# Kernel tuning notes

Measured on AMD Instinct MI355X. Metric: run time of the kernel, lower is better.

The kernel has to match this reference:

```python
import jax, jax.numpy as jnp
import numpy as np
from jax import lax

KERNELS = (3, 5, 7, 9, 11, 13, 15)
H = W = 4096


def _box_mean(x, k):
    """2D box-mean filter with replicate (edge) padding, computed separably.

    Edge padding is separable, so (pad2d -> kxk box) == (padH -> kx1 box -> padW -> 1xk box).
    x: [N, 1, H, W]
    """
    p = k // 2
    kh = jnp.full((1, 1, k, 1), 1.0 / k, dtype=x.dtype)
    kw = jnp.full((1, 1, 1, k), 1.0 / k, dtype=x.dtype)
    dn = ('NCHW', 'OIHW', 'NCHW')
    y = jnp.pad(x, ((0, 0), (0, 0), (p, p), (0, 0)), mode='edge')
    y = lax.conv_general_dilated(y, kh, (1, 1), 'VALID', dimension_numbers=dn)
    y = jnp.pad(y, ((0, 0), (0, 0), (0, 0), (p, p)), mode='edge')
    y = lax.conv_general_dilated(y, kw, (1, 1), 'VALID', dimension_numbers=dn)
    return y


def setup_inputs() -> dict:
    key = jax.random.key(0)
    k1, k2 = jax.random.split(key)
    x = jax.random.uniform(k1, (1, 1, H, W), dtype=jnp.float32)
    # binary occupancy-style map, as float (torch uses mapU8 -> fp16 multiply)
    map_mask = (jax.random.uniform(k2, (H, W)) > 0.5).astype(jnp.float32)
    return {"x": x, "map_mask": map_mask}


def reference(x, map_mask):
    # sum of 7 multi-scale box means, averaged, then masked by the map
    acc = _box_mean(x, KERNELS[0])
    for k in KERNELS[1:]:
        acc = acc + _box_mean(x, k)
    out = acc / len(KERNELS)
    return out * map_mask[None, None, :, :]
```

## Files before the change

kernel.cpp:

```cpp
#include <hip/hip_runtime.h>


#define TILE   64
#define HALO   7
#define LHX    8
#define NCOL   80
#define NROW   78
#define PSTR   83
#define PROWSA 81
#define HH     4096
#define WW     4096

__global__ __launch_bounds__(256, 8) void meanconv_kernel(
    const float* __restrict__ x, const float* __restrict__ mask,
    float* __restrict__ out)
{
    __shared__ float P[PROWSA * PSTR];
    const int tid = threadIdx.x;

    const int lid  = blockIdx.x;
    const int tile = ((lid & 7) << 9) | (lid >> 3);
    const int c0   = (tile & 63) * TILE;
    const int r0   = (tile >> 6) * TILE;

    const int g  = tid & 7;
    const int ty = tid >> 3;
    const int B0 = 8 * g;
    const size_t mrow0 = (size_t)(r0 + ty) * WW + c0 + B0;
    const size_t mrow1 = (size_t)(r0 + ty + 32) * WW + c0 + B0;
    float4 mk[4];
    mk[0] = *(const float4*)&mask[mrow0];
    mk[1] = *(const float4*)&mask[mrow0 + 4];
    mk[2] = *(const float4*)&mask[mrow1];
    mk[3] = *(const float4*)&mask[mrow1 + 4];

    if (tid < 81) P[tid] = 0.0f;

    const bool xint = (c0 >= LHX) && (c0 - LHX + NCOL <= WW);

    for (int idx = tid; idx < NROW * 4; idx += 256) {
        const int lr  = idx >> 2;
        const int s   = idx & 3;
        const int gr  = min(max(r0 + lr - HALO, 0), HH - 1);
        const int gc0 = c0 - LHX + 20 * s;
        float v[20];
        if (xint) {
            const float* src = &x[(size_t)gr * WW + gc0];
            #pragma unroll
            for (int q = 0; q < 5; ++q) {
                const float4 t = *(const float4*)(src + 4 * q);
                v[4*q+0] = t.x; v[4*q+1] = t.y; v[4*q+2] = t.z; v[4*q+3] = t.w;
            }
        } else {
            #pragma unroll
            for (int i = 0; i < 20; ++i) {
                const int gc = min(max(gc0 + i, 0), WW - 1);
                v[i] = x[(size_t)gr * WW + gc];
            }
        }
        #pragma unroll
        for (int i = 1; i < 20; ++i) v[i] += v[i - 1];
        const float tot = v[19];
        float sum = tot;
        float u = __shfl_up(sum, 1, 4); if (s >= 1) sum += u;
        u       = __shfl_up(sum, 2, 4); if (s >= 2) sum += u;
        const float off = sum - tot;
        float* dst = &P[(lr + 1) * PSTR + 1 + 20 * s];
        #pragma unroll
        for (int i = 0; i < 20; ++i) dst[i] = v[i] + off;
    }
    __syncthreads();

    for (int idx = tid; idx < 80 * 4; idx += 256) {
        const int c  = (idx >> 2) + 1;
        const int s  = idx & 3;
        const int rs = 1 + 20 * s;
        float v[20];
        float run = 0.0f;
        #pragma unroll
        for (int i = 0; i < 20; ++i) {
            const int r = rs + i;
            float t = P[r * PSTR + c];
            t = (r < 79) ? t : 0.0f;
            run += t; v[i] = run;
        }
        const float tot = run;
        float sum = tot;
        float u = __shfl_up(sum, 1, 4); if (s >= 1) sum += u;
        u       = __shfl_up(sum, 2, 4); if (s >= 2) sum += u;
        const float off = sum - tot;
        #pragma unroll
        for (int i = 0; i < 20; ++i) {
            const int r = rs + i;
            if (r < 79) P[r * PSTR + c] = v[i] + off;
        }
    }
    __syncthreads();

    #pragma unroll
    for (int j = 0; j < 2; ++j) {
        const int rr = ty + 32 * j;
        const int A  = rr + HALO;
        float a[8] = {0.f,0.f,0.f,0.f,0.f,0.f,0.f,0.f};
        #pragma unroll
        for (int p = 1; p <= 7; ++p) {
            const int   k = 2 * p + 1;
            const float w = 1.0f / (7.0f * (float)(k * k));
            const float* rT = &P[(A - p) * PSTR];
            const float* rB = &P[(A + p + 1) * PSTR];
            const int cl = B0 + LHX - p;
            const int cr = cl + 2 * p + 1;
            #pragma unroll
            for (int i = 0; i < 8; ++i) {
                a[i] += w * (rB[cr + i] - rT[cr + i] - rB[cl + i] + rT[cl + i]);
            }
        }
        const int gr = r0 + rr, gc = c0 + B0;
        const float4 m0 = mk[2 * j];
        const float4 m1 = mk[2 * j + 1];
        float4 o0, o1;
        o0.x = a[0] * m0.x; o0.y = a[1] * m0.y; o0.z = a[2] * m0.z; o0.w = a[3] * m0.w;
        o1.x = a[4] * m1.x; o1.y = a[5] * m1.y; o1.z = a[6] * m1.z; o1.w = a[7] * m1.w;
        *(float4*)&out[(size_t)gr * WW + gc]     = o0;
        *(float4*)&out[(size_t)gr * WW + gc + 4] = o1;
    }
}

extern "C" void kernel_launch(void* const* d_in, const int* in_sizes, int n_in,
                              void* d_out, int out_size, void* d_ws, size_t ws_size,
                              hipStream_t stream) {
    const float* x    = (const float*)d_in[0];
    const float* mask = (const float*)d_in[1];
    float*       out  = (float*)d_out;
    meanconv_kernel<<<dim3(64 * 64), 256, 0, stream>>>(x, mask, out);
}
```

Measured before the change: 207.1 us.

## Split integral-image scans into two segments per row/column and defer mask loads

The row and column prefix-sum passes switch from four 20-element segments per line to two 40/39-element segments. This drops one shuffle level and the loop striding, and shrinks the shared buffer by removing the leading zero column. The column pass recomputes from shared memory instead of holding a 20-element register array. Mask loads move from the kernel start to the epilogue, which lowers register pressure but exposes their latency and leaves fewer threads active during the scan phases.

```diff
diff --git a/kernel.cpp b/kernel.cpp
--- a/kernel.cpp
+++ b/kernel.cpp
@@ -7,7 +7,7 @@
 #define NCOL   80
 #define NROW   78
 #define PSTR   83
-#define PROWSA 81
+#define PROWS  79
 #define HH     4096
 #define WW     4096
 
@@ -15,7 +15,7 @@
     const float* __restrict__ x, const float* __restrict__ mask,
     float* __restrict__ out)
 {
-    __shared__ float P[PROWSA * PSTR];
+    __shared__ float P[PROWS * PSTR];
     const int tid = threadIdx.x;
 
     const int lid  = blockIdx.x;
@@ -23,80 +23,62 @@
     const int c0   = (tile & 63) * TILE;
     const int r0   = (tile >> 6) * TILE;
 
-    const int g  = tid & 7;
-    const int ty = tid >> 3;
-    const int B0 = 8 * g;
-    const size_t mrow0 = (size_t)(r0 + ty) * WW + c0 + B0;
-    const size_t mrow1 = (size_t)(r0 + ty + 32) * WW + c0 + B0;
-    float4 mk[4];
-    mk[0] = *(const float4*)&mask[mrow0];
-    mk[1] = *(const float4*)&mask[mrow0 + 4];
-    mk[2] = *(const float4*)&mask[mrow1];
-    mk[3] = *(const float4*)&mask[mrow1 + 4];
-
-    if (tid < 81) P[tid] = 0.0f;
+    if (tid < PSTR) P[tid] = 0.0f;
 
     const bool xint = (c0 >= LHX) && (c0 - LHX + NCOL <= WW);
 
-    for (int idx = tid; idx < NROW * 4; idx += 256) {
-        const int lr  = idx >> 2;
-        const int s   = idx & 3;
+    if (tid < NROW * 2) {
+        const int lr  = tid >> 1;
+        const int s   = tid & 1;
         const int gr  = min(max(r0 + lr - HALO, 0), HH - 1);
-        const int gc0 = c0 - LHX + 20 * s;
-        float v[20];
+        const int gc0 = c0 - LHX + 40 * s;
+        float v[40];
         if (xint) {
             const float* src = &x[(size_t)gr * WW + gc0];
             #pragma unroll
-            for (int q = 0; q < 5; ++q) {
+            for (int q = 0; q < 10; ++q) {
                 const float4 t = *(const float4*)(src + 4 * q);
                 v[4*q+0] = t.x; v[4*q+1] = t.y; v[4*q+2] = t.z; v[4*q+3] = t.w;
             }
         } else {
             #pragma unroll
-            for (int i = 0; i < 20; ++i) {
+            for (int i = 0; i < 40; ++i) {
                 const int gc = min(max(gc0 + i, 0), WW - 1);
                 v[i] = x[(size_t)gr * WW + gc];
             }
         }
         #pragma unroll
-        for (int i = 1; i < 20; ++i) v[i] += v[i - 1];
-        const float tot = v[19];
-        float sum = tot;
-        float u = __shfl_up(sum, 1, 4); if (s >= 1) sum += u;
-        u       = __shfl_up(sum, 2, 4); if (s >= 2) sum += u;
-        const float off = sum - tot;
-        float* dst = &P[(lr + 1) * PSTR + 1 + 20 * s];
+        for (int i = 1; i < 40; ++i) v[i] += v[i - 1];
+        const float tot = v[39];
+        const float u   = __shfl_up(tot, 1, 2);
+        const float off = (s == 1) ? u : 0.0f;
+        float* dst = &P[(lr + 1) * PSTR + 40 * s];
         #pragma unroll
-        for (int i = 0; i < 20; ++i) dst[i] = v[i] + off;
+        for (int i = 0; i < 40; ++i) dst[i] = v[i] + off;
     }
     __syncthreads();
 
-    for (int idx = tid; idx < 80 * 4; idx += 256) {
-        const int c  = (idx >> 2) + 1;
-        const int s  = idx & 3;
-        const int rs = 1 + 20 * s;
-        float v[20];
+    if (tid < NCOL * 2) {
+        const int c  = tid >> 1;
+        const int s  = tid & 1;
+        const int rs = 1 + 39 * s;
         float run = 0.0f;
         #pragma unroll
-        for (int i = 0; i < 20; ++i) {
-            const int r = rs + i;
-            float t = P[r * PSTR + c];
-            t = (r < 79) ? t : 0.0f;
-            run += t; v[i] = run;
-        }
-        const float tot = run;
-        float sum = tot;
-        float u = __shfl_up(sum, 1, 4); if (s >= 1) sum += u;
-        u       = __shfl_up(sum, 2, 4); if (s >= 2) sum += u;
-        const float off = sum - tot;
+        for (int i = 0; i < 39; ++i) run += P[(rs + i) * PSTR + c];
+        const float u   = __shfl_up(run, 1, 2);
+        const float off = (s == 1) ? u : 0.0f;
+        float acc = off;
         #pragma unroll
-        for (int i = 0; i < 20; ++i) {
-            const int r = rs + i;
-            if (r < 79) P[r * PSTR + c] = v[i] + off;
+        for (int i = 0; i < 39; ++i) {
+            acc += P[(rs + i) * PSTR + c];
+            P[(rs + i) * PSTR + c] = acc;
         }
     }
     __syncthreads();
 
+    const int g  = tid & 7;
+    const int ty = tid >> 3;
+    const int B0 = 8 * g;
     #pragma unroll
     for (int j = 0; j < 2; ++j) {
         const int rr = ty + 32 * j;
@@ -108,16 +90,16 @@
             const float w = 1.0f / (7.0f * (float)(k * k));
             const float* rT = &P[(A - p) * PSTR];
             const float* rB = &P[(A + p + 1) * PSTR];
-            const int cl = B0 + LHX - p;
-            const int cr = cl + 2 * p + 1;
+            const int cl = B0 + 7 - p;
+            const int cr = B0 + 8 + p;
             #pragma unroll
             for (int i = 0; i < 8; ++i) {
-                a[i] += w * (rB[cr + i] - rT[cr + i] - rB[cl + i] + rT[cl + i]);
+                a[i] += w * ((rB[cr + i] - rT[cr + i]) - (rB[cl + i] - rT[cl + i]));
             }
         }
         const int gr = r0 + rr, gc = c0 + B0;
-        const float4 m0 = mk[2 * j];
-        const float4 m1 = mk[2 * j + 1];
+        const float4 m0 = *(const float4*)&mask[(size_t)gr * WW + gc];
+        const float4 m1 = *(const float4*)&mask[(size_t)gr * WW + gc + 4];
         float4 o0, o1;
         o0.x = a[0] * m0.x; o0.y = a[1] * m0.y; o0.z = a[2] * m0.z; o0.w = a[3] * m0.w;
         o1.x = a[4] * m1.x; o1.y = a[5] * m1.y; o1.z = a[6] * m1.z; o1.w = a[7] * m1.w;
```

Measured after the change: 199.0 us. -3.9%, faster.
